# Optimization experiments

Measured on AMD Instinct MI355X. Metric: run time of the kernel, lower is better.

## Reference

```python
import jax, jax.numpy as jnp
import numpy as np

D_MODEL = 1024
NUM_HEADS = 16

def setup_inputs() -> dict:
    key = jax.random.key(0)
    k1, k2, k3 = jax.random.split(key, 3)
    scale = 1.0 / np.sqrt(D_MODEL)
    x = jax.random.normal(k1, (2, 2048, D_MODEL), dtype=jnp.float32)
    Wqkv = jax.random.normal(k2, (D_MODEL, 3 * D_MODEL), dtype=jnp.float32) * scale
    bqkv = jnp.zeros((3 * D_MODEL,), dtype=jnp.float32)
    Wout = jax.random.normal(k3, (D_MODEL, D_MODEL), dtype=jnp.float32) * scale
    bout = jnp.zeros((D_MODEL,), dtype=jnp.float32)
    return {"x": x, "Wqkv": Wqkv, "bqkv": bqkv, "Wout": Wout, "bout": bout}

def reference(x, Wqkv, bqkv, Wout, bout):
    B, T, d_model = x.shape
    H = NUM_HEADS
    d_k = d_model // H
    qkv = x @ Wqkv + bqkv                         # [B, T, 3*d_model]
    q, k, v = jnp.split(qkv, 3, axis=-1)
    def reshape(t):
        return t.reshape(B, T, H, d_k).transpose(0, 2, 1, 3)  # [B, H, T, d_k]
    q, k, v = map(reshape, (q, k, v))
    scores = jnp.einsum("bhqd,bhkd->bhqk", q, k) / jnp.sqrt(jnp.float32(d_k))
    attn = jax.nn.softmax(scores, axis=-1)        # [B, H, T, T]
    out = jnp.einsum("bhqk,bhkd->bhqd", attn, v)  # [B, H, T, d_k]
    out = out.transpose(0, 2, 1, 3).reshape(B, T, d_model)
    return out @ Wout + bout
```

## Files before the change

kernel.cpp:

```cpp
#include <hip/hip_runtime.h>
#include <stdint.h>

#define D_MODEL 1024
#define T_SEQ   2048
#define BATCH   2
#define NHEAD   16
#define DK      64

typedef short s16x8 __attribute__((ext_vector_type(8)));
typedef float f32x4 __attribute__((ext_vector_type(4)));

#define MFMA16(a, b, c) __builtin_amdgcn_mfma_f32_16x16x32_bf16((a), (b), (c), 0, 0, 0)

__device__ __forceinline__ unsigned short f2bf(float f) {
    union { float f; unsigned u; } v; v.f = f;
    unsigned r = v.u + 0x7fffu + ((v.u >> 16) & 1u);
    return (unsigned short)(r >> 16);
}

__global__ __launch_bounds__(256) void cast_x(const float* __restrict__ in,
                                              unsigned short* __restrict__ out, int n8) {
    int i = blockIdx.x * 256 + threadIdx.x;
    if (i >= n8) return;
    const float4* p = reinterpret_cast<const float4*>(in) + (size_t)i * 2;
    float4 a = p[0], b = p[1];
    union { s16x8 v; unsigned short u[8]; } o;
    o.u[0] = f2bf(a.x); o.u[1] = f2bf(a.y); o.u[2] = f2bf(a.z); o.u[3] = f2bf(a.w);
    o.u[4] = f2bf(b.x); o.u[5] = f2bf(b.y); o.u[6] = f2bf(b.z); o.u[7] = f2bf(b.w);
    reinterpret_cast<s16x8*>(out)[i] = o.v;
}

__global__ __launch_bounds__(256) void transpose_cast(const float* __restrict__ in,
                                                      unsigned short* __restrict__ out,
                                                      int R, int C) {
    __shared__ unsigned short tile[64][66];
    int c0 = blockIdx.x * 64, r0 = blockIdx.y * 64;
    int tid = threadIdx.x;
#pragma unroll
    for (int i = 0; i < 16; ++i) {
        int idx = tid + i * 256;
        int r = idx >> 6, c = idx & 63;
        tile[r][c] = f2bf(in[(size_t)(r0 + r) * C + c0 + c]);
    }
    __syncthreads();
#pragma unroll
    for (int i = 0; i < 16; ++i) {
        int idx = tid + i * 256;
        int cc = idx >> 6, rr = idx & 63;
        out[(size_t)(c0 + cc) * R + r0 + rr] = tile[rr][cc];
    }
}

__global__ __launch_bounds__(256) void transpose_v(const unsigned short* __restrict__ in,
                                                   unsigned short* __restrict__ out) {
    __shared__ unsigned short tile[64][66];
    int t0 = blockIdx.x * 64, bh = blockIdx.y;
    int tid = threadIdx.x;
    const unsigned short* src = in + (size_t)bh * T_SEQ * DK;
    unsigned short* dst = out + (size_t)bh * DK * T_SEQ;
#pragma unroll
    for (int i = 0; i < 16; ++i) {
        int idx = tid + i * 256;
        int tr = idx >> 6, d = idx & 63;
        tile[tr][d] = src[(size_t)(t0 + tr) * DK + d];
    }
    __syncthreads();
#pragma unroll
    for (int i = 0; i < 16; ++i) {
        int idx = tid + i * 256;
        int dd = idx >> 6, tt = idx & 63;
        dst[(size_t)dd * T_SEQ + t0 + tt] = tile[tt][dd];
    }
}

__device__ __forceinline__ void gload_lds16(const void* g, void* l) {
    __builtin_amdgcn_global_load_lds(
        (const __attribute__((address_space(1))) void*)g,
        (__attribute__((address_space(3))) void*)l, 16, 0, 0);
}

template <int EPI>
__global__ __launch_bounds__(256) void gemm_bt(
    const unsigned short* __restrict__ A, const unsigned short* __restrict__ Bt,
    int K, int N, const float* __restrict__ bias,
    float* __restrict__ outF,
    unsigned short* __restrict__ Qw, unsigned short* __restrict__ Kw,
    unsigned short* __restrict__ Vw) {
    __shared__ __align__(16) unsigned short lds[2][8192];
    const int tid = threadIdx.x;
    const int lane = tid & 63, wid = tid >> 6;
    const int g = lane >> 4, l15 = lane & 15;
    const int wm = wid >> 1, wn = wid & 1;
    const int mTile = blockIdx.y, nTile = blockIdx.x;
    const unsigned short* Ab = A + (size_t)mTile * 128 * K;
    const unsigned short* Bb = Bt + (size_t)nTile * 128 * K;
    const int srow = tid >> 2, schunk = (tid & 3) * 8;
    f32x4 acc[4][4] = {};

    auto stage = [&](int buf, int kt) {
        const unsigned short* ga = Ab + (size_t)srow * K + kt * 32 + schunk;
        const unsigned short* gb = Bb + (size_t)srow * K + kt * 32 + schunk;
        unsigned short* la = &lds[buf][tid * 8];
        unsigned short* lb = &lds[buf][4096 + tid * 8];
        gload_lds16(ga, la);
        gload_lds16(ga + (size_t)64 * K, la + 2048);
        gload_lds16(gb, lb);
        gload_lds16(gb + (size_t)64 * K, lb + 2048);
    };

    stage(0, 0);
    __syncthreads();
    const int nk = K >> 5;
    int buf = 0;
    for (int kt = 0; kt < nk; ++kt) {
        if (kt + 1 < nk) stage(buf ^ 1, kt + 1);
        const unsigned short* la = &lds[buf][0];
        const unsigned short* lb = &lds[buf][4096];
        s16x8 af[4], bfr[4];
#pragma unroll
        for (int m = 0; m < 4; ++m)
            af[m] = *(const s16x8*)&la[(wm * 64 + m * 16 + l15) * 32 + g * 8];
#pragma unroll
        for (int n = 0; n < 4; ++n)
            bfr[n] = *(const s16x8*)&lb[(wn * 64 + n * 16 + l15) * 32 + g * 8];
#pragma unroll
        for (int m = 0; m < 4; ++m)
#pragma unroll
            for (int n = 0; n < 4; ++n)
                acc[m][n] = MFMA16(af[m], bfr[n], acc[m][n]);
        __syncthreads();
        buf ^= 1;
    }

    const int rowBase = mTile * 128 + wm * 64;
    const int colBase = nTile * 128 + wn * 64;
#pragma unroll
    for (int m = 0; m < 4; ++m) {
#pragma unroll
        for (int n = 0; n < 4; ++n) {
            int col = colBase + n * 16 + l15;
            float bv = bias[col];
#pragma unroll
            for (int r = 0; r < 4; ++r) {
                int row = rowBase + m * 16 + 4 * g + r;
                float val = acc[m][n][r] + bv;
                if (EPI == 1) {
                    outF[(size_t)row * N + col] = val;
                } else {
                    int b = row >> 11, t = row & 2047;
                    if (col < 1024) {
                        int h = col >> 6, d = col & 63;
                        Qw[(((size_t)(b * NHEAD + h)) * T_SEQ + t) * DK + d] = f2bf(val * 0.125f);
                    } else if (col < 2048) {
                        int h = (col - 1024) >> 6, d = col & 63;
                        Kw[(((size_t)(b * NHEAD + h)) * T_SEQ + t) * DK + d] = f2bf(val);
                    } else {
                        int h = (col - 2048) >> 6, d = col & 63;
                        Vw[(((size_t)(b * NHEAD + h)) * T_SEQ + t) * DK + d] = f2bf(val);
                    }
                }
            }
        }
    }
}

__global__ __launch_bounds__(256) void attn_fwd(
    const unsigned short* __restrict__ Q, const unsigned short* __restrict__ Kx,
    const unsigned short* __restrict__ Vt, unsigned short* __restrict__ O) {
    __shared__ __align__(16) unsigned short Pl[4][16][72];
    const int tid = threadIdx.x;
    const int lane = tid & 63, wid = tid >> 6;
    const int g = lane >> 4, l15 = lane & 15;
    const int bh = blockIdx.y;
    const int b = bh >> 4, h = bh & 15;
    const int q0 = blockIdx.x * 128 + wid * 32;
    const unsigned short* Qh = Q + (size_t)bh * T_SEQ * DK;
    const unsigned short* Kh = Kx + (size_t)bh * T_SEQ * DK;
    const unsigned short* Vh = Vt + (size_t)bh * DK * T_SEQ;

    s16x8 qf[2][2];
#pragma unroll
    for (int qt = 0; qt < 2; ++qt)
#pragma unroll
        for (int dc = 0; dc < 2; ++dc)
            qf[qt][dc] = *(const s16x8*)&Qh[(size_t)(q0 + qt * 16 + l15) * DK + dc * 32 + g * 8];

    f32x4 o[2][4] = {};
    float mrun[2][4], lrun[2][4];
#pragma unroll
    for (int qt = 0; qt < 2; ++qt)
#pragma unroll
        for (int r = 0; r < 4; ++r) { mrun[qt][r] = -1e30f; lrun[qt][r] = 0.f; }

    for (int kv0 = 0; kv0 < T_SEQ; kv0 += 64) {
        s16x8 kf[4][2];
#pragma unroll
        for (int kq = 0; kq < 4; ++kq)
#pragma unroll
            for (int dc = 0; dc < 2; ++dc)
                kf[kq][dc] = *(const s16x8*)&Kh[(size_t)(kv0 + kq * 16 + l15) * DK + dc * 32 + g * 8];
        s16x8 vf[4][2];
#pragma unroll
        for (int dc16 = 0; dc16 < 4; ++dc16)
#pragma unroll
            for (int kc = 0; kc < 2; ++kc)
                vf[dc16][kc] = *(const s16x8*)&Vh[(size_t)(dc16 * 16 + l15) * T_SEQ + kv0 + kc * 32 + g * 8];

#pragma unroll
        for (int qt = 0; qt < 2; ++qt) {
            f32x4 s[4];
#pragma unroll
            for (int kq = 0; kq < 4; ++kq) {
                f32x4 z = {};
                z = MFMA16(qf[qt][0], kf[kq][0], z);
                z = MFMA16(qf[qt][1], kf[kq][1], z);
                s[kq] = z;
            }
            float tm[4];
#pragma unroll
            for (int r = 0; r < 4; ++r)
                tm[r] = fmaxf(fmaxf(s[0][r], s[1][r]), fmaxf(s[2][r], s[3][r]));
#pragma unroll
            for (int mask = 1; mask <= 8; mask <<= 1)
#pragma unroll
                for (int r = 0; r < 4; ++r)
                    tm[r] = fmaxf(tm[r], __shfl_xor(tm[r], mask));
            float sf[4];
#pragma unroll
            for (int r = 0; r < 4; ++r) {
                float mn = fmaxf(mrun[qt][r], tm[r]);
                sf[r] = __expf(mrun[qt][r] - mn);
                mrun[qt][r] = mn;
            }
            float p[4][4], ts[4];
#pragma unroll
            for (int r = 0; r < 4; ++r) ts[r] = 0.f;
#pragma unroll
            for (int kq = 0; kq < 4; ++kq)
#pragma unroll
                for (int r = 0; r < 4; ++r) {
                    p[kq][r] = __expf(s[kq][r] - mrun[qt][r]);
                    ts[r] += p[kq][r];
                }
#pragma unroll
            for (int r = 0; r < 4; ++r)
                lrun[qt][r] = lrun[qt][r] * sf[r] + ts[r];
#pragma unroll
            for (int dc16 = 0; dc16 < 4; ++dc16)
#pragma unroll
                for (int r = 0; r < 4; ++r)
                    o[qt][dc16][r] *= sf[r];
#pragma unroll
            for (int kq = 0; kq < 4; ++kq)
#pragma unroll
                for (int r = 0; r < 4; ++r)
                    Pl[wid][4 * g + r][kq * 16 + l15] = f2bf(p[kq][r]);
            s16x8 pf0 = *(const s16x8*)&Pl[wid][l15][g * 8];
            s16x8 pf1 = *(const s16x8*)&Pl[wid][l15][32 + g * 8];
#pragma unroll
            for (int dc16 = 0; dc16 < 4; ++dc16) {
                o[qt][dc16] = MFMA16(pf0, vf[dc16][0], o[qt][dc16]);
                o[qt][dc16] = MFMA16(pf1, vf[dc16][1], o[qt][dc16]);
            }
        }
    }

#pragma unroll
    for (int qt = 0; qt < 2; ++qt) {
#pragma unroll
        for (int mask = 1; mask <= 8; mask <<= 1)
#pragma unroll
            for (int r = 0; r < 4; ++r)
                lrun[qt][r] += __shfl_xor(lrun[qt][r], mask);
        float inv[4];
#pragma unroll
        for (int r = 0; r < 4; ++r) inv[r] = 1.f / lrun[qt][r];
#pragma unroll
        for (int dc16 = 0; dc16 < 4; ++dc16)
#pragma unroll
            for (int r = 0; r < 4; ++r) {
                int q = q0 + qt * 16 + 4 * g + r;
                O[((size_t)(b * T_SEQ + q)) * D_MODEL + h * DK + dc16 * 16 + l15] =
                    f2bf(o[qt][dc16][r] * inv[r]);
            }
    }
}

extern "C" void kernel_launch(void* const* d_in, const int* in_sizes, int n_in,
                              void* d_out, int out_size, void* d_ws, size_t ws_size,
                              hipStream_t stream) {
    const float* x    = (const float*)d_in[0];
    const float* Wqkv = (const float*)d_in[1];
    const float* bqkv = (const float*)d_in[2];
    const float* Wout = (const float*)d_in[3];
    const float* bout = (const float*)d_in[4];
    float* out = (float*)d_out;

    char* ws = (char*)d_ws;
    unsigned short* Xbf    = (unsigned short*)(ws + 0);
    unsigned short* WqkvT  = (unsigned short*)(ws + 8388608);
    unsigned short* WoutT  = (unsigned short*)(ws + 14680064);
    unsigned short* Qw     = (unsigned short*)(ws + 16777216);
    unsigned short* Kw     = (unsigned short*)(ws + 25165824);
    unsigned short* Vtmp   = (unsigned short*)(ws + 33554432);
    unsigned short* Vte    = (unsigned short*)(ws + 41943040);
    unsigned short* Ows    = (unsigned short*)(ws + 50331648);

    cast_x<<<2048, 256, 0, stream>>>(x, Xbf, (BATCH * T_SEQ * D_MODEL) / 8);
    transpose_cast<<<dim3(48, 16), 256, 0, stream>>>(Wqkv, WqkvT, 1024, 3072);
    transpose_cast<<<dim3(16, 16), 256, 0, stream>>>(Wout, WoutT, 1024, 1024);
    gemm_bt<0><<<dim3(24, 32), 256, 0, stream>>>(Xbf, WqkvT, 1024, 3072, bqkv,
                                                 nullptr, Qw, Kw, Vtmp);
    transpose_v<<<dim3(32, 32), 256, 0, stream>>>(Vtmp, Vte);
    attn_fwd<<<dim3(16, 32), 256, 0, stream>>>(Qw, Kw, Vte, Ows);
    gemm_bt<1><<<dim3(8, 32), 256, 0, stream>>>(Ows, WoutT, 1024, 1024, bout,
                                                out, nullptr, nullptr, nullptr);
}
```

Before: 269.5 us.

## Rewrite attention inner loop with 32x32 MFMA, transposed scores and lazy rescale

The attention kernel moves from 16x16x32 to 32x32x16 bf16 MFMA and computes S^T = K·Q^T, so each lane owns one query column. That turns the row max and sum into in-register reductions plus one cross-half shuffle. P is packed to bf16 in registers with v_cvt_pk_bf16 and v_permlane32_swap instead of a round trip through LDS. The output rescale is skipped unless the running max grows by more than 8, which saves exp and multiply work but lets unnormalised values grow by up to e^8 before correction.

```diff
diff --git a/kernel.cpp b/kernel.cpp
--- a/kernel.cpp
+++ b/kernel.cpp
@@ -9,13 +9,28 @@
 
 typedef short s16x8 __attribute__((ext_vector_type(8)));
 typedef float f32x4 __attribute__((ext_vector_type(4)));
+typedef float f32x16 __attribute__((ext_vector_type(16)));
 
 #define MFMA16(a, b, c) __builtin_amdgcn_mfma_f32_16x16x32_bf16((a), (b), (c), 0, 0, 0)
+#define MFMA32(a, b, c) __builtin_amdgcn_mfma_f32_32x32x16_bf16((a), (b), (c), 0, 0, 0)
+#define CROW(r) ((((r) & 3)) + 8 * ((r) >> 2))
 
 __device__ __forceinline__ unsigned short f2bf(float f) {
     union { float f; unsigned u; } v; v.f = f;
     unsigned r = v.u + 0x7fffu + ((v.u >> 16) & 1u);
     return (unsigned short)(r >> 16);
+}
+
+__device__ __forceinline__ unsigned cvtpk_bf16(float lo, float hi) {
+    unsigned r;
+    asm("v_cvt_pk_bf16_f32 %0, %1, %2" : "=v"(r) : "v"(lo), "v"(hi));
+    return r;
+}
+
+__device__ __forceinline__ float bperm_f(int srclane, float v) {
+    int iv = __builtin_bit_cast(int, v);
+    int r = __builtin_amdgcn_ds_bpermute(srclane << 2, iv);
+    return __builtin_bit_cast(float, r);
 }
 
 __global__ __launch_bounds__(256) void cast_x(const float* __restrict__ in,
@@ -167,10 +182,9 @@
 __global__ __launch_bounds__(256) void attn_fwd(
     const unsigned short* __restrict__ Q, const unsigned short* __restrict__ Kx,
     const unsigned short* __restrict__ Vt, unsigned short* __restrict__ O) {
-    __shared__ __align__(16) unsigned short Pl[4][16][72];
     const int tid = threadIdx.x;
     const int lane = tid & 63, wid = tid >> 6;
-    const int g = lane >> 4, l15 = lane & 15;
+    const int l31 = lane & 31, hi = lane >> 5;
     const int bh = blockIdx.y;
     const int b = bh >> 4, h = bh & 15;
     const int q0 = blockIdx.x * 128 + wid * 32;
@@ -178,111 +192,91 @@
     const unsigned short* Kh = Kx + (size_t)bh * T_SEQ * DK;
     const unsigned short* Vh = Vt + (size_t)bh * DK * T_SEQ;
 
-    s16x8 qf[2][2];
-#pragma unroll
-    for (int qt = 0; qt < 2; ++qt)
-#pragma unroll
-        for (int dc = 0; dc < 2; ++dc)
-            qf[qt][dc] = *(const s16x8*)&Qh[(size_t)(q0 + qt * 16 + l15) * DK + dc * 32 + g * 8];
-
-    f32x4 o[2][4] = {};
-    float mrun[2][4], lrun[2][4];
-#pragma unroll
-    for (int qt = 0; qt < 2; ++qt)
-#pragma unroll
-        for (int r = 0; r < 4; ++r) { mrun[qt][r] = -1e30f; lrun[qt][r] = 0.f; }
+    s16x8 qf[4];
+#pragma unroll
+    for (int dt = 0; dt < 4; ++dt)
+        qf[dt] = *(const s16x8*)&Qh[(size_t)(q0 + l31) * DK + dt * 16 + hi * 8];
+
+    f32x16 o0 = {}, o1 = {};
+    float m = -1e30f, lr = 0.f;
 
     for (int kv0 = 0; kv0 < T_SEQ; kv0 += 64) {
-        s16x8 kf[4][2];
-#pragma unroll
-        for (int kq = 0; kq < 4; ++kq)
-#pragma unroll
-            for (int dc = 0; dc < 2; ++dc)
-                kf[kq][dc] = *(const s16x8*)&Kh[(size_t)(kv0 + kq * 16 + l15) * DK + dc * 32 + g * 8];
-        s16x8 vf[4][2];
-#pragma unroll
-        for (int dc16 = 0; dc16 < 4; ++dc16)
-#pragma unroll
-            for (int kc = 0; kc < 2; ++kc)
-                vf[dc16][kc] = *(const s16x8*)&Vh[(size_t)(dc16 * 16 + l15) * T_SEQ + kv0 + kc * 32 + g * 8];
-
-#pragma unroll
-        for (int qt = 0; qt < 2; ++qt) {
-            f32x4 s[4];
-#pragma unroll
-            for (int kq = 0; kq < 4; ++kq) {
-                f32x4 z = {};
-                z = MFMA16(qf[qt][0], kf[kq][0], z);
-                z = MFMA16(qf[qt][1], kf[kq][1], z);
-                s[kq] = z;
-            }
-            float tm[4];
-#pragma unroll
-            for (int r = 0; r < 4; ++r)
-                tm[r] = fmaxf(fmaxf(s[0][r], s[1][r]), fmaxf(s[2][r], s[3][r]));
-#pragma unroll
-            for (int mask = 1; mask <= 8; mask <<= 1)
-#pragma unroll
-                for (int r = 0; r < 4; ++r)
-                    tm[r] = fmaxf(tm[r], __shfl_xor(tm[r], mask));
-            float sf[4];
-#pragma unroll
-            for (int r = 0; r < 4; ++r) {
-                float mn = fmaxf(mrun[qt][r], tm[r]);
-                sf[r] = __expf(mrun[qt][r] - mn);
-                mrun[qt][r] = mn;
-            }
-            float p[4][4], ts[4];
-#pragma unroll
-            for (int r = 0; r < 4; ++r) ts[r] = 0.f;
-#pragma unroll
-            for (int kq = 0; kq < 4; ++kq)
-#pragma unroll
-                for (int r = 0; r < 4; ++r) {
-                    p[kq][r] = __expf(s[kq][r] - mrun[qt][r]);
-                    ts[r] += p[kq][r];
-                }
-#pragma unroll
-            for (int r = 0; r < 4; ++r)
-                lrun[qt][r] = lrun[qt][r] * sf[r] + ts[r];
-#pragma unroll
-            for (int dc16 = 0; dc16 < 4; ++dc16)
-#pragma unroll
-                for (int r = 0; r < 4; ++r)
-                    o[qt][dc16][r] *= sf[r];
-#pragma unroll
-            for (int kq = 0; kq < 4; ++kq)
-#pragma unroll
-                for (int r = 0; r < 4; ++r)
-                    Pl[wid][4 * g + r][kq * 16 + l15] = f2bf(p[kq][r]);
-            s16x8 pf0 = *(const s16x8*)&Pl[wid][l15][g * 8];
-            s16x8 pf1 = *(const s16x8*)&Pl[wid][l15][32 + g * 8];
-#pragma unroll
-            for (int dc16 = 0; dc16 < 4; ++dc16) {
-                o[qt][dc16] = MFMA16(pf0, vf[dc16][0], o[qt][dc16]);
-                o[qt][dc16] = MFMA16(pf1, vf[dc16][1], o[qt][dc16]);
+        s16x8 kf[2][4];
+#pragma unroll
+        for (int kt = 0; kt < 2; ++kt)
+#pragma unroll
+            for (int dt = 0; dt < 4; ++dt)
+                kf[kt][dt] = *(const s16x8*)&Kh[(size_t)(kv0 + kt * 32 + l31) * DK + dt * 16 + hi * 8];
+        s16x8 vf[2][4];
+#pragma unroll
+        for (int dt2 = 0; dt2 < 2; ++dt2)
+#pragma unroll
+            for (int ks = 0; ks < 4; ++ks)
+                vf[dt2][ks] = *(const s16x8*)&Vh[(size_t)(dt2 * 32 + l31) * T_SEQ + kv0 + ks * 16 + hi * 8];
+
+        f32x16 p[2] = {};
+#pragma unroll
+        for (int kt = 0; kt < 2; ++kt)
+#pragma unroll
+            for (int dt = 0; dt < 4; ++dt)
+                p[kt] = MFMA32(kf[kt][dt], qf[dt], p[kt]);
+
+        float tm = p[0][0];
+#pragma unroll
+        for (int r = 1; r < 16; ++r) tm = fmaxf(tm, p[0][r]);
+#pragma unroll
+        for (int r = 0; r < 16; ++r) tm = fmaxf(tm, p[1][r]);
+        tm = fmaxf(tm, __shfl_xor(tm, 32));
+
+        if (!__all(tm <= m + 8.0f)) {
+            float mn = fmaxf(m, tm);
+            float sf = __expf(m - mn);
+            lr *= sf;
+            m = mn;
+            float sfr;
+#pragma unroll
+            for (int r = 0; r < 16; ++r) {
+                sfr = bperm_f(CROW(r) + 4 * hi, sf);
+                o0[r] *= sfr; o1[r] *= sfr;
             }
         }
-    }
-
-#pragma unroll
-    for (int qt = 0; qt < 2; ++qt) {
-#pragma unroll
-        for (int mask = 1; mask <= 8; mask <<= 1)
-#pragma unroll
-            for (int r = 0; r < 4; ++r)
-                lrun[qt][r] += __shfl_xor(lrun[qt][r], mask);
-        float inv[4];
-#pragma unroll
-        for (int r = 0; r < 4; ++r) inv[r] = 1.f / lrun[qt][r];
-#pragma unroll
-        for (int dc16 = 0; dc16 < 4; ++dc16)
-#pragma unroll
-            for (int r = 0; r < 4; ++r) {
-                int q = q0 + qt * 16 + 4 * g + r;
-                O[((size_t)(b * T_SEQ + q)) * D_MODEL + h * DK + dc16 * 16 + l15] =
-                    f2bf(o[qt][dc16][r] * inv[r]);
+
+        float ts = 0.f;
+#pragma unroll
+        for (int kt = 0; kt < 2; ++kt)
+#pragma unroll
+            for (int r = 0; r < 16; ++r) {
+                float e = __expf(p[kt][r] - m);
+                p[kt][r] = e;
+                ts += e;
             }
+        lr += ts;
+
+#pragma unroll
+        for (int ks = 0; ks < 4; ++ks) {
+            const int kt = ks >> 1, rb = (ks & 1) * 8;
+            unsigned w0 = cvtpk_bf16(p[kt][rb + 0], p[kt][rb + 1]);
+            unsigned w2 = cvtpk_bf16(p[kt][rb + 4], p[kt][rb + 5]);
+            asm volatile("v_permlane32_swap_b32 %0, %1" : "+v"(w0), "+v"(w2));
+            unsigned w1 = cvtpk_bf16(p[kt][rb + 2], p[kt][rb + 3]);
+            unsigned w3 = cvtpk_bf16(p[kt][rb + 6], p[kt][rb + 7]);
+            asm volatile("v_permlane32_swap_b32 %0, %1" : "+v"(w1), "+v"(w3));
+            union { unsigned w[4]; s16x8 v; } pu;
+            pu.w[0] = w0; pu.w[1] = w1; pu.w[2] = w2; pu.w[3] = w3;
+            o0 = MFMA32(pu.v, vf[0][ks], o0);
+            o1 = MFMA32(pu.v, vf[1][ks], o1);
+        }
+    }
+
+    lr += __shfl_xor(lr, 32);
+    float li = 1.f / lr;
+#pragma unroll
+    for (int r = 0; r < 16; ++r) {
+        float lir = bperm_f(CROW(r) + 4 * hi, li);
+        int q = q0 + CROW(r) + 4 * hi;
+        size_t base = ((size_t)(b * T_SEQ + q)) * D_MODEL + h * DK;
+        O[base + l31]      = f2bf(o0[r] * lir);
+        O[base + 32 + l31] = f2bf(o1[r] * lir);
     }
 }
 
```

After: 266.1 us. Within noise of the previous version (-1.3%).
